# Kernel optimization log

Hardware: AMD Instinct MI355X
Metric: run time of the kernel (lower is better)

The kernel has to match this reference:

```python
import jax, jax.numpy as jnp
import numpy as np

CLIP = 50.0
EPS = 1e-8


def _attn_jacobian_agg(q, k, v, scale):
    """Aggregate attention Jacobian dO/dq summed over queries, plus attention outputs.

    q: (B, Q, d); k, v: (B, S, d).
    Per-query Jacobian: J_q = scale * sum_j p_j v_j (k_j - kbar)^T, kbar = sum_i p_i k_i.
    Returns (agg_jac: (B, d, d), outputs: (B, Q, d)).
    """
    scores = jnp.einsum('bqd,bsd->bqs', q, k) * scale
    p = jax.nn.softmax(scores, axis=-1)
    out = jnp.einsum('bqs,bsd->bqd', p, v)           # attention outputs O
    kbar = jnp.einsum('bqs,bsd->bqd', p, k)          # expected key per query
    # sum_j p_j v_j k_j^T  -> (B, Q, d, d)
    pvk = jnp.einsum('bqs,bsd,bse->bqde', p, v, k)
    jac = scale * (pvk - out[..., :, None] * kbar[..., None, :])
    return jac.sum(axis=1), out


def setup_inputs() -> dict:
    key = jax.random.key(0)
    ks = jax.random.split(key, 5)
    B, Q, S, M, D = 256, 16, 512, 8, 128
    return {
        'queries': jax.random.normal(ks[0], (B, Q, D), dtype=jnp.float32),
        'keys':    jax.random.normal(ks[1], (B, S, D), dtype=jnp.float32),
        'values':  jax.random.normal(ks[2], (B, S, D), dtype=jnp.float32),
        'k_cg':    jax.random.normal(ks[3], (B, M, D), dtype=jnp.float32),
        'v_cg':    jax.random.normal(ks[4], (B, M, D), dtype=jnp.float32),
    }


def reference(queries, keys, values, k_cg, v_cg):
    B, Q, d = queries.shape
    scale = d ** -0.5

    dense_jac, dense_out = _attn_jacobian_agg(queries, keys, values, scale)
    cg_jac, cg_out = _attn_jacobian_agg(queries, k_cg, v_cg, scale)

    # jacobian_clip_value = 50.0 (config default)
    dense_jac = jnp.clip(dense_jac, -CLIP, CLIP)
    cg_jac = jnp.clip(cg_jac, -CLIP, CLIP)

    df = dense_jac.reshape(B, -1)
    cf = cg_jac.reshape(B, -1)
    dn = jnp.linalg.norm(df, axis=-1)
    cn = jnp.linalg.norm(cf, axis=-1)
    cosine_sim = (df * cf).sum(axis=-1) / (dn * cn + EPS)
    force_direction_loss = 1.0 - cosine_sim

    # consistency: per-query output MSE, averaged over queries, scaled by 1/d_head
    out_diff = dense_out - cg_out
    per_query_mse = (out_diff ** 2).sum(axis=-1)          # (B, Q)
    consistency_loss = per_query_mse.sum(axis=-1) / Q / d  # (B,)

    # v4 loss: L = w_dir * L_force_cos + w_cons * L_consistency (defaults 1.0, 1.0)
    total = 1.0 * force_direction_loss + 1.0 * consistency_loss
    return total.mean()  # reduction='mean'
```

## Files before the change

### kernel.cpp

```cpp
#include <hip/hip_runtime.h>
#include <math.h>


namespace {
constexpr int Bn = 256, Qn = 16, Sn = 512, Mn = 8, Dn = 128;
constexpr int NT = 512;
constexpr float SCALE = 0.08838834764831845f;
constexpr float CLIPV = 50.0f;

constexpr int QS    = 0;
constexpr int PB    = 4352;
constexpr int WOFF  = 20992;
constexpr int ARENA = 23040;
constexpr int KT    = ARENA;
constexpr int VT    = ARENA + 18432;
constexpr int VTW   = ARENA + 27648;
constexpr int SCF   = ARENA;
constexpr int CGS   = 59904;
constexpr int PCG   = 60416;
constexpr int WC    = 61696;
constexpr int RED   = 61728;
constexpr int LDSZ  = 61856;

typedef __attribute__((ext_vector_type(8))) short bf16x8;
typedef __attribute__((ext_vector_type(4))) float f32x4;
#define MFMA16(a, b, c) __builtin_amdgcn_mfma_f32_16x16x32_bf16((a), (b), (c), 0, 0, 0)

__device__ inline unsigned int pack2t(float a, float b) {
  return __builtin_amdgcn_perm(__builtin_bit_cast(unsigned int, b),
                               __builtin_bit_cast(unsigned int, a), 0x07060302u);
}
__device__ inline unsigned short f2bf(float x) {
  unsigned int u = __builtin_bit_cast(unsigned int, x);
  u += 0x7fffu + ((u >> 16) & 1u);
  return (unsigned short)(u >> 16);
}
__device__ inline float bf2f(unsigned short h) {
  unsigned int u = ((unsigned int)h) << 16;
  return __builtin_bit_cast(float, u);
}
union Frag {
  bf16x8 v;
  unsigned int u[4];
  unsigned short h[8];
};

__global__ void zero_ws_kernel(float4* ws) {
  ws[threadIdx.x] = make_float4(0.f, 0.f, 0.f, 0.f);
}

__global__ void finalize_kernel(const float* __restrict__ ws, float* __restrict__ out) {
  __shared__ float sr[256];
  int i = threadIdx.x;
  float dt = ws[i * 4 + 0], n1 = ws[i * 4 + 1], n2 = ws[i * 4 + 2], cs = ws[i * 4 + 3];
  float cosv = dt / (sqrtf(n1) * sqrtf(n2) + 1e-8f);
  sr[i] = (1.0f - cosv) + cs * (1.0f / (float)(Qn * Dn));
  __syncthreads();
  for (int off = 128; off; off >>= 1) {
    if (i < off) sr[i] += sr[i + off];
    __syncthreads();
  }
  if (i == 0) out[0] = sr[0] * (1.0f / (float)Bn);
}

__global__ __launch_bounds__(NT, 4) void fm_kernel(
    const float* __restrict__ Qg, const float* __restrict__ Kg,
    const float* __restrict__ Vg, const float* __restrict__ Kcg,
    const float* __restrict__ Vcg, float* __restrict__ ws) {
  __shared__ __align__(16) char L[LDSZ];
  const int bid = blockIdx.x, b = bid & 255, h = bid >> 8;
  const int t = threadIdx.x, lane = t & 63, wv = t >> 6;
  const int quad = lane >> 4, l16 = lane & 15;

  const float* Qb = Qg + (size_t)b * Qn * Dn;
  const float* Kb = Kg + (size_t)b * Sn * Dn;
  const float* Vb = Vg + (size_t)b * Sn * Dn;
  const float* Kc = Kcg + (size_t)b * Mn * Dn;
  const float* Vc = Vcg + (size_t)b * Mn * Dn;

  const int dK = t & 127, gK = t >> 7;
  const int dV = t & 63, gV = t >> 6;
  float kpf[2][8], vpf[8];

  auto load_tiles = [&](int st) {
#pragma unroll
    for (int o = 0; o < 2; ++o) {
      int s0 = st * 64 + (gK + 4 * o) * 8;
#pragma unroll
      for (int i = 0; i < 8; ++i) kpf[o][i] = Kb[(size_t)(s0 + i) * Dn + dK];
    }
    int s1 = st * 64 + gV * 8;
#pragma unroll
    for (int i = 0; i < 8; ++i) vpf[i] = Vb[(size_t)(s1 + i) * Dn + h * 64 + dV];
  };
  auto store_tiles = [&](int st) {
#pragma unroll
    for (int o = 0; o < 2; ++o) {
      unsigned int u0 = pack2t(kpf[o][0], kpf[o][1]), u1 = pack2t(kpf[o][2], kpf[o][3]);
      unsigned int u2 = pack2t(kpf[o][4], kpf[o][5]), u3 = pack2t(kpf[o][6], kpf[o][7]);
      *(uint4*)(L + KT + dK * 144 + (gK + 4 * o) * 16) = make_uint4(u0, u1, u2, u3);
    }
    int s1 = st * 64 + gV * 8;
    float4 wlo = *(const float4*)(L + WOFF + s1 * 4);
    float4 whi = *(const float4*)(L + WOFF + s1 * 4 + 16);
    float wv8[8] = {wlo.x, wlo.y, wlo.z, wlo.w, whi.x, whi.y, whi.z, whi.w};
    unsigned int v0 = pack2t(vpf[0], vpf[1]), v1 = pack2t(vpf[2], vpf[3]);
    unsigned int v2 = pack2t(vpf[4], vpf[5]), v3 = pack2t(vpf[6], vpf[7]);
    *(uint4*)(L + VT + dV * 144 + gV * 16) = make_uint4(v0, v1, v2, v3);
    unsigned int w0 = pack2t(wv8[0] * vpf[0], wv8[1] * vpf[1]);
    unsigned int w1 = pack2t(wv8[2] * vpf[2], wv8[3] * vpf[3]);
    unsigned int w2 = pack2t(wv8[4] * vpf[4], wv8[5] * vpf[5]);
    unsigned int w3 = pack2t(wv8[6] * vpf[6], wv8[7] * vpf[7]);
    *(uint4*)(L + VTW + dV * 144 + gV * 16) = make_uint4(w0, w1, w2, w3);
  };

  {
    int row = t >> 5, c4 = t & 31;
    float4 qv = ((const float4*)Qb)[t];
    unsigned int p0 = pack2t(qv.x * SCALE, qv.y * SCALE);
    unsigned int p1 = pack2t(qv.z * SCALE, qv.w * SCALE);
    *(unsigned long long*)(L + QS + row * 272 + c4 * 8) =
        (unsigned long long)p0 | ((unsigned long long)p1 << 32);
  }
  load_tiles(0);
  __syncthreads();

  {
    bf16x8 aq[4];
#pragma unroll
    for (int kk = 0; kk < 4; ++kk)
      aq[kk] = *(const bf16x8*)(L + QS + l16 * 272 + kk * 64 + quad * 16);
    for (int j = 0; j < 4; ++j) {
      int srow = 64 * wv + 16 * j + l16;
      const float* kp = Kb + (size_t)srow * Dn + quad * 8;
      f32x4 acc = {0.f, 0.f, 0.f, 0.f};
#pragma unroll
      for (int kk = 0; kk < 4; ++kk) {
        float4 lo = *(const float4*)(kp + kk * 32);
        float4 hi = *(const float4*)(kp + kk * 32 + 4);
        Frag f;
        f.u[0] = pack2t(lo.x, lo.y);
        f.u[1] = pack2t(lo.z, lo.w);
        f.u[2] = pack2t(hi.x, hi.y);
        f.u[3] = pack2t(hi.z, hi.w);
        acc = MFMA16(aq[kk], f.v, acc);
      }
      int s = 64 * wv + 16 * j + l16;
#pragma unroll
      for (int r = 0; r < 4; ++r)
        *(float*)(L + SCF + (quad * 4 + r) * 2064 + s * 4) = acc[r];
    }
  }
  __syncthreads();

#pragma unroll
  for (int rr = 0; rr < 2; ++rr) {
    int q = wv * 2 + rr;
    const float* srow = (const float*)(L + SCF + q * 2064);
    float x[8];
    float m = -1e30f;
#pragma unroll
    for (int i = 0; i < 8; ++i) { x[i] = srow[lane * 8 + i]; m = fmaxf(m, x[i]); }
#pragma unroll
    for (int o = 32; o; o >>= 1) m = fmaxf(m, __shfl_xor(m, o));
    float ssum = 0.f;
#pragma unroll
    for (int i = 0; i < 8; ++i) { x[i] = __expf(x[i] - m); ssum += x[i]; }
#pragma unroll
    for (int o = 32; o; o >>= 1) ssum += __shfl_xor(ssum, o);
    float inv = 1.f / ssum;
    Frag g;
#pragma unroll
    for (int i = 0; i < 8; ++i) g.h[i] = f2bf(x[i] * inv);
    *(bf16x8*)(L + PB + q * 1040 + lane * 16) = g.v;
  }
  __syncthreads();
  {
    float wsv = 0.f;
#pragma unroll
    for (int q = 0; q < Qn; ++q)
      wsv += bf2f(*(const unsigned short*)(L + PB + q * 1040 + t * 2));
    *(float*)(L + WOFF + t * 4) = wsv;
  }
  __syncthreads();

  const int rp = wv & 1, ch = wv >> 1;
  f32x4 C00 = {0.f,0.f,0.f,0.f}, C01 = {0.f,0.f,0.f,0.f};
  f32x4 C10 = {0.f,0.f,0.f,0.f}, C11 = {0.f,0.f,0.f,0.f};
  f32x4 outacc = {0.f,0.f,0.f,0.f}, kbacc = {0.f,0.f,0.f,0.f};

  auto ckstep = [&](int colByte, f32x4& c00, f32x4& c01, f32x4& c10, f32x4& c11) {
    bf16x8 A0 = *(const bf16x8*)(L + VTW + (rp * 32 + l16) * 144 + colByte + quad * 16);
    bf16x8 A1 = *(const bf16x8*)(L + VTW + (rp * 32 + 16 + l16) * 144 + colByte + quad * 16);
    bf16x8 B0 = *(const bf16x8*)(L + KT + (ch * 32 + l16) * 144 + colByte + quad * 16);
    bf16x8 B1 = *(const bf16x8*)(L + KT + (ch * 32 + 16 + l16) * 144 + colByte + quad * 16);
    c00 = MFMA16(A0, B0, c00);
    c01 = MFMA16(A0, B1, c01);
    c10 = MFMA16(A1, B0, c10);
    c11 = MFMA16(A1, B1, c11);
  };

  for (int st = 0; st < 8; ++st) {
    if (st) __syncthreads();
    store_tiles(st);
    __syncthreads();
    if (st < 7) load_tiles(st + 1);
#pragma unroll
    for (int z = 0; z < 2; ++z) {
      int colByte = z * 64;
      bf16x8 pA = *(const bf16x8*)(L + PB + l16 * 1040 + st * 128 + z * 64 + quad * 16);
      bf16x8 bK = *(const bf16x8*)(L + KT + (wv * 16 + l16) * 144 + colByte + quad * 16);
      kbacc = MFMA16(pA, bK, kbacc);
      if (wv < 4) {
        bf16x8 bV = *(const bf16x8*)(L + VT + (wv * 16 + l16) * 144 + colByte + quad * 16);
        outacc = MFMA16(pA, bV, outacc);
      }
      ckstep(colByte, C00, C01, C10, C11);
    }
  }
  __syncthreads();

  if (wv < 4) {
#pragma unroll
    for (int r = 0; r < 4; ++r)
      *(unsigned short*)(L + VTW + (wv * 16 + l16) * 144 + (quad * 4 + r) * 2) = f2bf(-outacc[r]);
  }
#pragma unroll
  for (int r = 0; r < 4; ++r)
    *(unsigned short*)(L + KT + (wv * 16 + l16) * 144 + (quad * 4 + r) * 2) = f2bf(kbacc[r]);
  if (t < 256) {
    *(uint4*)(L + KT + (t >> 1) * 144 + 32 + (t & 1) * 16) = make_uint4(0, 0, 0, 0);
  } else if (t < 384) {
    int i = t - 256;
    *(uint4*)(L + VTW + (i >> 1) * 144 + 32 + (i & 1) * 16) = make_uint4(0, 0, 0, 0);
  }
  __syncthreads();
  ckstep(0, C00, C01, C10, C11);
#pragma unroll
  for (int r = 0; r < 4; ++r) {
    C00[r] = fminf(fmaxf(SCALE * C00[r], -CLIPV), CLIPV);
    C01[r] = fminf(fmaxf(SCALE * C01[r], -CLIPV), CLIPV);
    C10[r] = fminf(fmaxf(SCALE * C10[r], -CLIPV), CLIPV);
    C11[r] = fminf(fmaxf(SCALE * C11[r], -CLIPV), CLIPV);
  }
  __syncthreads();

  if (wv == 0) {
    f32x4 acc = {0.f, 0.f, 0.f, 0.f};
    const float* kp = Kc + (size_t)(l16 & 7) * Dn + quad * 8;
#pragma unroll
    for (int kk = 0; kk < 4; ++kk) {
      bf16x8 a = *(const bf16x8*)(L + QS + l16 * 272 + kk * 64 + quad * 16);
      float4 lo = *(const float4*)(kp + kk * 32);
      float4 hi = *(const float4*)(kp + kk * 32 + 4);
      Frag f;
      f.u[0] = pack2t(lo.x, lo.y);
      f.u[1] = pack2t(lo.z, lo.w);
      f.u[2] = pack2t(hi.x, hi.y);
      f.u[3] = pack2t(hi.z, hi.w);
      acc = MFMA16(a, f.v, acc);
    }
    if (l16 < 8) {
#pragma unroll
      for (int r = 0; r < 4; ++r)
        *(float*)(L + CGS + (quad * 4 + r) * 32 + l16 * 4) = acc[r];
    }
  }
  __syncthreads();
  if (t < 16) {
    float xs[8];
    float m = -1e30f;
#pragma unroll
    for (int s = 0; s < 8; ++s) { xs[s] = *(const float*)(L + CGS + t * 32 + s * 4); m = fmaxf(m, xs[s]); }
    float ssum = 0.f;
#pragma unroll
    for (int s = 0; s < 8; ++s) { xs[s] = __expf(xs[s] - m); ssum += xs[s]; }
    float inv = 1.f / ssum;
#pragma unroll
    for (int s = 0; s < 4; ++s)
      *(unsigned int*)(L + PCG + t * 80 + s * 4) = pack2t(xs[2 * s] * inv, xs[2 * s + 1] * inv);
#pragma unroll
    for (int p = 4; p < 16; ++p) *(unsigned int*)(L + PCG + t * 80 + p * 4) = 0u;
  }
  __syncthreads();
  if (t < 8) {
    float s = 0.f;
#pragma unroll
    for (int q = 0; q < Qn; ++q) s += bf2f(*(const unsigned short*)(L + PCG + q * 80 + t * 2));
    *(float*)(L + WC + t * 4) = s;
  }
  __syncthreads();
  if (t < 128) {
    float kv[8];
#pragma unroll
    for (int i = 0; i < 8; ++i) kv[i] = Kc[(size_t)i * Dn + t];
    *(uint4*)(L + KT + t * 144) = make_uint4(pack2t(kv[0], kv[1]), pack2t(kv[2], kv[3]),
                                             pack2t(kv[4], kv[5]), pack2t(kv[6], kv[7]));
    *(uint4*)(L + KT + t * 144 + 16) = make_uint4(0, 0, 0, 0);
    *(uint4*)(L + KT + t * 144 + 32) = make_uint4(0, 0, 0, 0);
    *(uint4*)(L + KT + t * 144 + 48) = make_uint4(0, 0, 0, 0);
  } else if (t < 192) {
    int d = t - 128;
    float vv2[8];
#pragma unroll
    for (int i = 0; i < 8; ++i) vv2[i] = Vc[(size_t)i * Dn + h * 64 + d];
    *(uint4*)(L + VT + d * 144) = make_uint4(pack2t(vv2[0], vv2[1]), pack2t(vv2[2], vv2[3]),
                                             pack2t(vv2[4], vv2[5]), pack2t(vv2[6], vv2[7]));
    *(uint4*)(L + VT + d * 144 + 16) = make_uint4(0, 0, 0, 0);
    *(uint4*)(L + VT + d * 144 + 32) = make_uint4(0, 0, 0, 0);
    *(uint4*)(L + VT + d * 144 + 48) = make_uint4(0, 0, 0, 0);
  } else if (t < 256) {
    int d = t - 192;
    float vv2[8], wcv[8];
#pragma unroll
    for (int i = 0; i < 8; ++i) {
      vv2[i] = Vc[(size_t)i * Dn + h * 64 + d];
      wcv[i] = *(const float*)(L + WC + i * 4);
    }
    *(uint4*)(L + VTW + d * 144) =
        make_uint4(pack2t(wcv[0] * vv2[0], wcv[1] * vv2[1]), pack2t(wcv[2] * vv2[2], wcv[3] * vv2[3]),
                   pack2t(wcv[4] * vv2[4], wcv[5] * vv2[5]), pack2t(wcv[6] * vv2[6], wcv[7] * vv2[7]));
    *(uint4*)(L + VTW + d * 144 + 16) = make_uint4(0, 0, 0, 0);
    *(uint4*)(L + VTW + d * 144 + 32) = make_uint4(0, 0, 0, 0);
    *(uint4*)(L + VTW + d * 144 + 48) = make_uint4(0, 0, 0, 0);
  }
  __syncthreads();
  f32x4 outc = {0.f,0.f,0.f,0.f}, kbc = {0.f,0.f,0.f,0.f};
  f32x4 D00 = {0.f,0.f,0.f,0.f}, D01 = {0.f,0.f,0.f,0.f};
  f32x4 D10 = {0.f,0.f,0.f,0.f}, D11 = {0.f,0.f,0.f,0.f};
  {
    bf16x8 pA = *(const bf16x8*)(L + PCG + l16 * 80 + quad * 16);
    bf16x8 bK = *(const bf16x8*)(L + KT + (wv * 16 + l16) * 144 + quad * 16);
    kbc = MFMA16(pA, bK, kbc);
    if (wv < 4) {
      bf16x8 bV = *(const bf16x8*)(L + VT + (wv * 16 + l16) * 144 + quad * 16);
      outc = MFMA16(pA, bV, outc);
    }
    ckstep(0, D00, D01, D10, D11);
  }
  __syncthreads();
  if (wv < 4) {
#pragma unroll
    for (int r = 0; r < 4; ++r)
      *(unsigned short*)(L + VTW + (wv * 16 + l16) * 144 + (quad * 4 + r) * 2) = f2bf(-outc[r]);
  }
#pragma unroll
  for (int r = 0; r < 4; ++r)
    *(unsigned short*)(L + KT + (wv * 16 + l16) * 144 + (quad * 4 + r) * 2) = f2bf(kbc[r]);
  __syncthreads();
  ckstep(0, D00, D01, D10, D11);
#pragma unroll
  for (int r = 0; r < 4; ++r) {
    D00[r] = fminf(fmaxf(SCALE * D00[r], -CLIPV), CLIPV);
    D01[r] = fminf(fmaxf(SCALE * D01[r], -CLIPV), CLIPV);
    D10[r] = fminf(fmaxf(SCALE * D10[r], -CLIPV), CLIPV);
    D11[r] = fminf(fmaxf(SCALE * D11[r], -CLIPV), CLIPV);
  }

  float dot = 0.f, nd2 = 0.f, nc2 = 0.f, cons = 0.f;
#pragma unroll
  for (int r = 0; r < 4; ++r) {
    dot += C00[r] * D00[r] + C01[r] * D01[r] + C10[r] * D10[r] + C11[r] * D11[r];
    nd2 += C00[r] * C00[r] + C01[r] * C01[r] + C10[r] * C10[r] + C11[r] * C11[r];
    nc2 += D00[r] * D00[r] + D01[r] * D01[r] + D10[r] * D10[r] + D11[r] * D11[r];
  }
  if (wv < 4) {
#pragma unroll
    for (int r = 0; r < 4; ++r) {
      float df = outacc[r] - outc[r];
      cons += df * df;
    }
  }
#pragma unroll
  for (int o = 32; o; o >>= 1) {
    dot += __shfl_xor(dot, o);
    nd2 += __shfl_xor(nd2, o);
    nc2 += __shfl_xor(nc2, o);
    cons += __shfl_xor(cons, o);
  }
  if (lane == 0) {
    float* red = (float*)(L + RED);
    red[wv * 4 + 0] = dot;
    red[wv * 4 + 1] = nd2;
    red[wv * 4 + 2] = nc2;
    red[wv * 4 + 3] = cons;
  }
  __syncthreads();
  if (t == 0) {
    const float* red = (const float*)(L + RED);
    float d_ = 0.f, n1 = 0.f, n2 = 0.f, cs = 0.f;
#pragma unroll
    for (int w = 0; w < 8; ++w) {
      d_ += red[w * 4 + 0];
      n1 += red[w * 4 + 1];
      n2 += red[w * 4 + 2];
      cs += red[w * 4 + 3];
    }
    atomicAdd(ws + b * 4 + 0, d_);
    atomicAdd(ws + b * 4 + 1, n1);
    atomicAdd(ws + b * 4 + 2, n2);
    atomicAdd(ws + b * 4 + 3, cs);
  }
}
}

extern "C" void kernel_launch(void* const* d_in, const int* in_sizes, int n_in,
                              void* d_out, int out_size, void* d_ws, size_t ws_size,
                              hipStream_t stream) {
  const float* q = (const float*)d_in[0];
  const float* k = (const float*)d_in[1];
  const float* v = (const float*)d_in[2];
  const float* kc = (const float*)d_in[3];
  const float* vc = (const float*)d_in[4];
  float* out = (float*)d_out;
  float* ws = (float*)d_ws;
  zero_ws_kernel<<<1, 256, 0, stream>>>((float4*)ws);
  fm_kernel<<<2 * Bn, NT, 0, stream>>>(q, k, v, kc, vc, ws);
  finalize_kernel<<<1, 256, 0, stream>>>(ws, out);
}
```

Baseline: 174.2 us.

## Shrink LDS footprint with register softmax and 32-row tiles for higher occupancy

The softmax now runs on the score MFMA accumulators held in registers. Cross-wave max and sum reductions go through small LDS scratch areas, which removes the large score staging buffer and its extra passes. The S-dimension tiles shrink from 64 to 32 rows (16 pipeline steps, 80-byte row stride), so LDS drops from about 62KB to about 46KB and launch bounds rise to 6 blocks per CU. Block-to-batch mapping changes so both head halves of a batch are adjacent, improving L2 reuse. In exchange there are more barriers per block and twice as many loop iterations.

```diff
diff --git a/kernel.cpp b/kernel.cpp
--- a/kernel.cpp
+++ b/kernel.cpp
@@ -8,19 +8,19 @@
 constexpr float SCALE = 0.08838834764831845f;
 constexpr float CLIPV = 50.0f;
 
-constexpr int QS    = 0;
-constexpr int PB    = 4352;
-constexpr int WOFF  = 20992;
-constexpr int ARENA = 23040;
-constexpr int KT    = ARENA;
-constexpr int VT    = ARENA + 18432;
-constexpr int VTW   = ARENA + 27648;
-constexpr int SCF   = ARENA;
-constexpr int CGS   = 59904;
-constexpr int PCG   = 60416;
-constexpr int WC    = 61696;
-constexpr int RED   = 61728;
-constexpr int LDSZ  = 61856;
+constexpr int QS   = 0;
+constexpr int PB   = 4352;
+constexpr int WOFF = 20992;
+constexpr int SMX0 = 23040;
+constexpr int SMX1 = 23552;
+constexpr int KT   = 24064;
+constexpr int VT   = 34304;
+constexpr int VTW  = 39424;
+constexpr int CGS  = 44544;
+constexpr int PCG  = 45056;
+constexpr int WC   = 46336;
+constexpr int RED  = 46368;
+constexpr int LDSZ = 46496;
 
 typedef __attribute__((ext_vector_type(8))) short bf16x8;
 typedef __attribute__((ext_vector_type(4))) float f32x4;
@@ -63,12 +63,12 @@
   if (i == 0) out[0] = sr[0] * (1.0f / (float)Bn);
 }
 
-__global__ __launch_bounds__(NT, 4) void fm_kernel(
+__global__ __launch_bounds__(NT, 6) void fm_kernel(
     const float* __restrict__ Qg, const float* __restrict__ Kg,
     const float* __restrict__ Vg, const float* __restrict__ Kcg,
     const float* __restrict__ Vcg, float* __restrict__ ws) {
   __shared__ __align__(16) char L[LDSZ];
-  const int bid = blockIdx.x, b = bid & 255, h = bid >> 8;
+  const int bid = blockIdx.x, b = bid >> 1, h = bid & 1;
   const int t = threadIdx.x, lane = t & 63, wv = t >> 6;
   const int quad = lane >> 4, l16 = lane & 15;
 
@@ -79,39 +79,38 @@
   const float* Vc = Vcg + (size_t)b * Mn * Dn;
 
   const int dK = t & 127, gK = t >> 7;
-  const int dV = t & 63, gV = t >> 6;
-  float kpf[2][8], vpf[8];
+  const int dV = t & 63, gV = (t >> 6) & 3;
+  const bool vrole = t < 256;
+  float kpf[8], vpf[8];
 
   auto load_tiles = [&](int st) {
-#pragma unroll
-    for (int o = 0; o < 2; ++o) {
-      int s0 = st * 64 + (gK + 4 * o) * 8;
-#pragma unroll
-      for (int i = 0; i < 8; ++i) kpf[o][i] = Kb[(size_t)(s0 + i) * Dn + dK];
-    }
-    int s1 = st * 64 + gV * 8;
-#pragma unroll
-    for (int i = 0; i < 8; ++i) vpf[i] = Vb[(size_t)(s1 + i) * Dn + h * 64 + dV];
+    int s0 = st * 32 + gK * 8;
+#pragma unroll
+    for (int i = 0; i < 8; ++i) kpf[i] = Kb[(size_t)(s0 + i) * Dn + dK];
+    if (vrole) {
+      int s1 = st * 32 + gV * 8;
+#pragma unroll
+      for (int i = 0; i < 8; ++i) vpf[i] = Vb[(size_t)(s1 + i) * Dn + h * 64 + dV];
+    }
   };
   auto store_tiles = [&](int st) {
-#pragma unroll
-    for (int o = 0; o < 2; ++o) {
-      unsigned int u0 = pack2t(kpf[o][0], kpf[o][1]), u1 = pack2t(kpf[o][2], kpf[o][3]);
-      unsigned int u2 = pack2t(kpf[o][4], kpf[o][5]), u3 = pack2t(kpf[o][6], kpf[o][7]);
-      *(uint4*)(L + KT + dK * 144 + (gK + 4 * o) * 16) = make_uint4(u0, u1, u2, u3);
-    }
-    int s1 = st * 64 + gV * 8;
-    float4 wlo = *(const float4*)(L + WOFF + s1 * 4);
-    float4 whi = *(const float4*)(L + WOFF + s1 * 4 + 16);
-    float wv8[8] = {wlo.x, wlo.y, wlo.z, wlo.w, whi.x, whi.y, whi.z, whi.w};
-    unsigned int v0 = pack2t(vpf[0], vpf[1]), v1 = pack2t(vpf[2], vpf[3]);
-    unsigned int v2 = pack2t(vpf[4], vpf[5]), v3 = pack2t(vpf[6], vpf[7]);
-    *(uint4*)(L + VT + dV * 144 + gV * 16) = make_uint4(v0, v1, v2, v3);
-    unsigned int w0 = pack2t(wv8[0] * vpf[0], wv8[1] * vpf[1]);
-    unsigned int w1 = pack2t(wv8[2] * vpf[2], wv8[3] * vpf[3]);
-    unsigned int w2 = pack2t(wv8[4] * vpf[4], wv8[5] * vpf[5]);
-    unsigned int w3 = pack2t(wv8[6] * vpf[6], wv8[7] * vpf[7]);
-    *(uint4*)(L + VTW + dV * 144 + gV * 16) = make_uint4(w0, w1, w2, w3);
+    unsigned int u0 = pack2t(kpf[0], kpf[1]), u1 = pack2t(kpf[2], kpf[3]);
+    unsigned int u2 = pack2t(kpf[4], kpf[5]), u3 = pack2t(kpf[6], kpf[7]);
+    *(uint4*)(L + KT + dK * 80 + gK * 16) = make_uint4(u0, u1, u2, u3);
+    if (vrole) {
+      int s1 = st * 32 + gV * 8;
+      float4 wlo = *(const float4*)(L + WOFF + s1 * 4);
+      float4 whi = *(const float4*)(L + WOFF + s1 * 4 + 16);
+      float wv8[8] = {wlo.x, wlo.y, wlo.z, wlo.w, whi.x, whi.y, whi.z, whi.w};
+      unsigned int v0 = pack2t(vpf[0], vpf[1]), v1 = pack2t(vpf[2], vpf[3]);
+      unsigned int v2 = pack2t(vpf[4], vpf[5]), v3 = pack2t(vpf[6], vpf[7]);
+      *(uint4*)(L + VT + dV * 80 + gV * 16) = make_uint4(v0, v1, v2, v3);
+      unsigned int w0 = pack2t(wv8[0] * vpf[0], wv8[1] * vpf[1]);
+      unsigned int w1 = pack2t(wv8[2] * vpf[2], wv8[3] * vpf[3]);
+      unsigned int w2 = pack2t(wv8[4] * vpf[4], wv8[5] * vpf[5]);
+      unsigned int w3 = pack2t(wv8[6] * vpf[6], wv8[7] * vpf[7]);
+      *(uint4*)(L + VTW + dV * 80 + gV * 16) = make_uint4(w0, w1, w2, w3);
+    }
   };
 
   {
@@ -122,17 +121,17 @@
     *(unsigned long long*)(L + QS + row * 272 + c4 * 8) =
         (unsigned long long)p0 | ((unsigned long long)p1 << 32);
   }
-  load_tiles(0);
-  __syncthreads();
-
+  __syncthreads();
+
+  float sc[4][4];
   {
     bf16x8 aq[4];
 #pragma unroll
     for (int kk = 0; kk < 4; ++kk)
       aq[kk] = *(const bf16x8*)(L + QS + l16 * 272 + kk * 64 + quad * 16);
+#pragma unroll
     for (int j = 0; j < 4; ++j) {
-      int srow = 64 * wv + 16 * j + l16;
-      const float* kp = Kb + (size_t)srow * Dn + quad * 8;
+      const float* kp = Kb + (size_t)(64 * wv + 16 * j + l16) * Dn + quad * 8;
       f32x4 acc = {0.f, 0.f, 0.f, 0.f};
 #pragma unroll
       for (int kk = 0; kk < 4; ++kk) {
@@ -145,42 +144,79 @@
         f.u[3] = pack2t(hi.z, hi.w);
         acc = MFMA16(aq[kk], f.v, acc);
       }
+#pragma unroll
+      for (int r = 0; r < 4; ++r) sc[j][r] = acc[r];
+    }
+  }
+  load_tiles(0);
+
+  {
+    float pm[4];
+#pragma unroll
+    for (int r = 0; r < 4; ++r)
+      pm[r] = fmaxf(fmaxf(sc[0][r], sc[1][r]), fmaxf(sc[2][r], sc[3][r]));
+#pragma unroll
+    for (int o = 8; o; o >>= 1) {
+#pragma unroll
+      for (int r = 0; r < 4; ++r) pm[r] = fmaxf(pm[r], __shfl_xor(pm[r], o));
+    }
+    if (l16 == 0) {
+#pragma unroll
+      for (int r = 0; r < 4; ++r)
+        *(float*)(L + SMX0 + ((quad * 4 + r) * 8 + wv) * 4) = pm[r];
+    }
+    __syncthreads();
+    float gm[4];
+#pragma unroll
+    for (int r = 0; r < 4; ++r) {
+      int q = quad * 4 + r;
+      float4 a = *(const float4*)(L + SMX0 + q * 32);
+      float4 c = *(const float4*)(L + SMX0 + q * 32 + 16);
+      gm[r] = fmaxf(fmaxf(fmaxf(a.x, a.y), fmaxf(a.z, a.w)),
+                    fmaxf(fmaxf(c.x, c.y), fmaxf(c.z, c.w)));
+    }
+    float ps[4] = {0.f, 0.f, 0.f, 0.f};
+#pragma unroll
+    for (int j = 0; j < 4; ++j) {
+#pragma unroll
+      for (int r = 0; r < 4; ++r) {
+        sc[j][r] = __expf(sc[j][r] - gm[r]);
+        ps[r] += sc[j][r];
+      }
+    }
+#pragma unroll
+    for (int o = 8; o; o >>= 1) {
+#pragma unroll
+      for (int r = 0; r < 4; ++r) ps[r] += __shfl_xor(ps[r], o);
+    }
+    if (l16 == 0) {
+#pragma unroll
+      for (int r = 0; r < 4; ++r)
+        *(float*)(L + SMX1 + ((quad * 4 + r) * 8 + wv) * 4) = ps[r];
+    }
+    __syncthreads();
+    float inv[4];
+#pragma unroll
+    for (int r = 0; r < 4; ++r) {
+      int q = quad * 4 + r;
+      float4 a = *(const float4*)(L + SMX1 + q * 32);
+      float4 c = *(const float4*)(L + SMX1 + q * 32 + 16);
+      inv[r] = 1.f / (a.x + a.y + a.z + a.w + c.x + c.y + c.z + c.w);
+    }
+#pragma unroll
+    for (int j = 0; j < 4; ++j) {
       int s = 64 * wv + 16 * j + l16;
-#pragma unroll
-      for (int r = 0; r < 4; ++r)
-        *(float*)(L + SCF + (quad * 4 + r) * 2064 + s * 4) = acc[r];
-    }
-  }
-  __syncthreads();
-
-#pragma unroll
-  for (int rr = 0; rr < 2; ++rr) {
-    int q = wv * 2 + rr;
-    const float* srow = (const float*)(L + SCF + q * 2064);
-    float x[8];
-    float m = -1e30f;
-#pragma unroll
-    for (int i = 0; i < 8; ++i) { x[i] = srow[lane * 8 + i]; m = fmaxf(m, x[i]); }
-#pragma unroll
-    for (int o = 32; o; o >>= 1) m = fmaxf(m, __shfl_xor(m, o));
-    float ssum = 0.f;
-#pragma unroll
-    for (int i = 0; i < 8; ++i) { x[i] = __expf(x[i] - m); ssum += x[i]; }
-#pragma unroll
-    for (int o = 32; o; o >>= 1) ssum += __shfl_xor(ssum, o);
-    float inv = 1.f / ssum;
-    Frag g;
-#pragma unroll
-    for (int i = 0; i < 8; ++i) g.h[i] = f2bf(x[i] * inv);
-    *(bf16x8*)(L + PB + q * 1040 + lane * 16) = g.v;
-  }
-  __syncthreads();
-  {
-    float wsv = 0.f;
-#pragma unroll
-    for (int q = 0; q < Qn; ++q)
-      wsv += bf2f(*(const unsigned short*)(L + PB + q * 1040 + t * 2));
-    *(float*)(L + WOFF + t * 4) = wsv;
+      float wpart = 0.f;
+#pragma unroll
+      for (int r = 0; r < 4; ++r) {
+        float p = sc[j][r] * inv[r];
+        *(unsigned short*)(L + PB + (quad * 4 + r) * 1040 + s * 2) = f2bf(p);
+        wpart += p;
+      }
+      wpart += __shfl_xor(wpart, 16);
+      wpart += __shfl_xor(wpart, 32);
+      if (quad == j) *(float*)(L + WOFF + s * 4) = wpart;
+    }
   }
   __syncthreads();
 
@@ -189,53 +225,49 @@
   f32x4 C10 = {0.f,0.f,0.f,0.f}, C11 = {0.f,0.f,0.f,0.f};
   f32x4 outacc = {0.f,0.f,0.f,0.f}, kbacc = {0.f,0.f,0.f,0.f};
 
-  auto ckstep = [&](int colByte, f32x4& c00, f32x4& c01, f32x4& c10, f32x4& c11) {
-    bf16x8 A0 = *(const bf16x8*)(L + VTW + (rp * 32 + l16) * 144 + colByte + quad * 16);
-    bf16x8 A1 = *(const bf16x8*)(L + VTW + (rp * 32 + 16 + l16) * 144 + colByte + quad * 16);
-    bf16x8 B0 = *(const bf16x8*)(L + KT + (ch * 32 + l16) * 144 + colByte + quad * 16);
-    bf16x8 B1 = *(const bf16x8*)(L + KT + (ch * 32 + 16 + l16) * 144 + colByte + quad * 16);
+  auto ckstep = [&](f32x4& c00, f32x4& c01, f32x4& c10, f32x4& c11) {
+    bf16x8 A0 = *(const bf16x8*)(L + VTW + (rp * 32 + l16) * 80 + quad * 16);
+    bf16x8 A1 = *(const bf16x8*)(L + VTW + (rp * 32 + 16 + l16) * 80 + quad * 16);
+    bf16x8 B0 = *(const bf16x8*)(L + KT + (ch * 32 + l16) * 80 + quad * 16);
+    bf16x8 B1 = *(const bf16x8*)(L + KT + (ch * 32 + 16 + l16) * 80 + quad * 16);
     c00 = MFMA16(A0, B0, c00);
     c01 = MFMA16(A0, B1, c01);
     c10 = MFMA16(A1, B0, c10);
     c11 = MFMA16(A1, B1, c11);
   };
 
-  for (int st = 0; st < 8; ++st) {
+  for (int st = 0; st < 16; ++st) {
     if (st) __syncthreads();
     store_tiles(st);
     __syncthreads();
-    if (st < 7) load_tiles(st + 1);
-#pragma unroll
-    for (int z = 0; z < 2; ++z) {
-      int colByte = z * 64;
-      bf16x8 pA = *(const bf16x8*)(L + PB + l16 * 1040 + st * 128 + z * 64 + quad * 16);
-      bf16x8 bK = *(const bf16x8*)(L + KT + (wv * 16 + l16) * 144 + colByte + quad * 16);
-      kbacc = MFMA16(pA, bK, kbacc);
-      if (wv < 4) {
-        bf16x8 bV = *(const bf16x8*)(L + VT + (wv * 16 + l16) * 144 + colByte + quad * 16);
-        outacc = MFMA16(pA, bV, outacc);
-      }
-      ckstep(colByte, C00, C01, C10, C11);
-    }
+    if (st < 15) load_tiles(st + 1);
+    bf16x8 pA = *(const bf16x8*)(L + PB + l16 * 1040 + st * 64 + quad * 16);
+    bf16x8 bK = *(const bf16x8*)(L + KT + (wv * 16 + l16) * 80 + quad * 16);
+    kbacc = MFMA16(pA, bK, kbacc);
+    if (wv < 4) {
+      bf16x8 bV = *(const bf16x8*)(L + VT + (wv * 16 + l16) * 80 + quad * 16);
+      outacc = MFMA16(pA, bV, outacc);
+    }
+    ckstep(C00, C01, C10, C11);
   }
   __syncthreads();
 
   if (wv < 4) {
 #pragma unroll
     for (int r = 0; r < 4; ++r)
-      *(unsigned short*)(L + VTW + (wv * 16 + l16) * 144 + (quad * 4 + r) * 2) = f2bf(-outacc[r]);
+      *(unsigned short*)(L + VTW + (wv * 16 + l16) * 80 + (quad * 4 + r) * 2) = f2bf(-outacc[r]);
   }
 #pragma unroll
   for (int r = 0; r < 4; ++r)
-    *(unsigned short*)(L + KT + (wv * 16 + l16) * 144 + (quad * 4 + r) * 2) = f2bf(kbacc[r]);
+    *(unsigned short*)(L + KT + (wv * 16 + l16) * 80 + (quad * 4 + r) * 2) = f2bf(kbacc[r]);
   if (t < 256) {
-    *(uint4*)(L + KT + (t >> 1) * 144 + 32 + (t & 1) * 16) = make_uint4(0, 0, 0, 0);
+    *(uint4*)(L + KT + (t >> 1) * 80 + 32 + (t & 1) * 16) = make_uint4(0, 0, 0, 0);
   } else if (t < 384) {
     int i = t - 256;
-    *(uint4*)(L + VTW + (i >> 1) * 144 + 32 + (i & 1) * 16) = make_uint4(0, 0, 0, 0);
-  }
-  __syncthreads();
-  ckstep(0, C00, C01, C10, C11);
+    *(uint4*)(L + VTW + (i >> 1) * 80 + 32 + (i & 1) * 16) = make_uint4(0, 0, 0, 0);
+  }
+  __syncthreads();
+  ckstep(C00, C01, C10, C11);
 #pragma unroll
   for (int r = 0; r < 4; ++r) {
     C00[r] = fminf(fmaxf(SCALE * C00[r], -CLIPV), CLIPV);
@@ -294,21 +326,21 @@
     float kv[8];
 #pragma unroll
     for (int i = 0; i < 8; ++i) kv[i] = Kc[(size_t)i * Dn + t];
-    *(uint4*)(L + KT + t * 144) = make_uint4(pack2t(kv[0], kv[1]), pack2t(kv[2], kv[3]),
-                                             pack2t(kv[4], kv[5]), pack2t(kv[6], kv[7]));
-    *(uint4*)(L + KT + t * 144 + 16) = make_uint4(0, 0, 0, 0);
-    *(uint4*)(L + KT + t * 144 + 32) = make_uint4(0, 0, 0, 0);
-    *(uint4*)(L + KT + t * 144 + 48) = make_uint4(0, 0, 0, 0);
+    *(uint4*)(L + KT + t * 80) = make_uint4(pack2t(kv[0], kv[1]), pack2t(kv[2], kv[3]),
+                                            pack2t(kv[4], kv[5]), pack2t(kv[6], kv[7]));
+    *(uint4*)(L + KT + t * 80 + 16) = make_uint4(0, 0, 0, 0);
+    *(uint4*)(L + KT + t * 80 + 32) = make_uint4(0, 0, 0, 0);
+    *(uint4*)(L + KT + t * 80 + 48) = make_uint4(0, 0, 0, 0);
   } else if (t < 192) {
     int d = t - 128;
     float vv2[8];
 #pragma unroll
     for (int i = 0; i < 8; ++i) vv2[i] = Vc[(size_t)i * Dn + h * 64 + d];
-    *(uint4*)(L + VT + d * 144) = make_uint4(pack2t(vv2[0], vv2[1]), pack2t(vv2[2], vv2[3]),
-                                             pack2t(vv2[4], vv2[5]), pack2t(vv2[6], vv2[7]));
-    *(uint4*)(L + VT + d * 144 + 16) = make_uint4(0, 0, 0, 0);
-    *(uint4*)(L + VT + d * 144 + 32) = make_uint4(0, 0, 0, 0);
-    *(uint4*)(L + VT + d * 144 + 48) = make_uint4(0, 0, 0, 0);
+    *(uint4*)(L + VT + d * 80) = make_uint4(pack2t(vv2[0], vv2[1]), pack2t(vv2[2], vv2[3]),
+                                            pack2t(vv2[4], vv2[5]), pack2t(vv2[6], vv2[7]));
+    *(uint4*)(L + VT + d * 80 + 16) = make_uint4(0, 0, 0, 0);
+    *(uint4*)(L + VT + d * 80 + 32) = make_uint4(0, 0, 0, 0);
+    *(uint4*)(L + VT + d * 80 + 48) = make_uint4(0, 0, 0, 0);
   } else if (t < 256) {
     int d = t - 192;
     float vv2[8], wcv[8];
@@ -317,12 +349,12 @@
       vv2[i] = Vc[(size_t)i * Dn + h * 64 + d];
       wcv[i] = *(const float*)(L + WC + i * 4);
     }
-    *(uint4*)(L + VTW + d * 144) =
+    *(uint4*)(L + VTW + d * 80) =
         make_uint4(pack2t(wcv[0] * vv2[0], wcv[1] * vv2[1]), pack2t(wcv[2] * vv2[2], wcv[3] * vv2[3]),
                    pack2t(wcv[4] * vv2[4], wcv[5] * vv2[5]), pack2t(wcv[6] * vv2[6], wcv[7] * vv2[7]));
-    *(uint4*)(L + VTW + d * 144 + 16) = make_uint4(0, 0, 0, 0);
-    *(uint4*)(L + VTW + d * 144 + 32) = make_uint4(0, 0, 0, 0);
-    *(uint4*)(L + VTW + d * 144 + 48) = make_uint4(0, 0, 0, 0);
+    *(uint4*)(L + VTW + d * 80 + 16) = make_uint4(0, 0, 0, 0);
+    *(uint4*)(L + VTW + d * 80 + 32) = make_uint4(0, 0, 0, 0);
+    *(uint4*)(L + VTW + d * 80 + 48) = make_uint4(0, 0, 0, 0);
   }
   __syncthreads();
   f32x4 outc = {0.f,0.f,0.f,0.f}, kbc = {0.f,0.f,0.f,0.f};
@@ -330,25 +362,25 @@
   f32x4 D10 = {0.f,0.f,0.f,0.f}, D11 = {0.f,0.f,0.f,0.f};
   {
     bf16x8 pA = *(const bf16x8*)(L + PCG + l16 * 80 + quad * 16);
-    bf16x8 bK = *(const bf16x8*)(L + KT + (wv * 16 + l16) * 144 + quad * 16);
+    bf16x8 bK = *(const bf16x8*)(L + KT + (wv * 16 + l16) * 80 + quad * 16);
     kbc = MFMA16(pA, bK, kbc);
     if (wv < 4) {
-      bf16x8 bV = *(const bf16x8*)(L + VT + (wv * 16 + l16) * 144 + quad * 16);
+      bf16x8 bV = *(const bf16x8*)(L + VT + (wv * 16 + l16) * 80 + quad * 16);
       outc = MFMA16(pA, bV, outc);
     }
-    ckstep(0, D00, D01, D10, D11);
+    ckstep(D00, D01, D10, D11);
   }
   __syncthreads();
   if (wv < 4) {
 #pragma unroll
     for (int r = 0; r < 4; ++r)
-      *(unsigned short*)(L + VTW + (wv * 16 + l16) * 144 + (quad * 4 + r) * 2) = f2bf(-outc[r]);
+      *(unsigned short*)(L + VTW + (wv * 16 + l16) * 80 + (quad * 4 + r) * 2) = f2bf(-outc[r]);
   }
 #pragma unroll
   for (int r = 0; r < 4; ++r)
-    *(unsigned short*)(L + KT + (wv * 16 + l16) * 144 + (quad * 4 + r) * 2) = f2bf(kbc[r]);
-  __syncthreads();
-  ckstep(0, D00, D01, D10, D11);
+    *(unsigned short*)(L + KT + (wv * 16 + l16) * 80 + (quad * 4 + r) * 2) = f2bf(kbc[r]);
+  __syncthreads();
+  ckstep(D00, D01, D10, D11);
 #pragma unroll
   for (int r = 0; r < 4; ++r) {
     D00[r] = fminf(fmaxf(SCALE * D00[r], -CLIPV), CLIPV);
```

New measurement: 181.2 us. 4.0% more time.
